# Kernel optimization log

Hardware: AMD Instinct MI355X
Metric: run time of the kernel (lower is better)

Reference implementation:

```python
import jax, jax.numpy as jnp
import numpy as np

GROUP = 32  # group_size from init


def setup_inputs() -> dict:
    key = jax.random.key(0)
    k1, k2, k3, k4, k5 = jax.random.split(key, 5)
    O, K = 4096, 4096
    B, S = 2, 2048
    num_groups = K // GROUP
    x = jax.random.normal(k1, (B, S, K), dtype=jnp.float32)
    # packed uint8 bytes (two 4-bit values per byte), stored as int32
    weight_packed = jax.random.randint(k2, (O, K // 2), 0, 256, dtype=jnp.int32)
    # realistic small positive scales and zero-points in [0, 15]
    scales = jax.random.uniform(k3, (O, num_groups), dtype=jnp.float32) * 0.02 + 1e-4
    zero_points = jax.random.uniform(k4, (O, num_groups), dtype=jnp.float32) * 15.0
    bias = jax.random.normal(k5, (O,), dtype=jnp.float32)
    return {"x": x, "weight_packed": weight_packed, "scales": scales,
            "zero_points": zero_points, "bias": bias}


def reference(x, weight_packed, scales, zero_points, bias):
    O, Kh = weight_packed.shape
    # unpack 4-bit values: even input index -> low nibble, odd -> high nibble
    low = weight_packed & 15
    high = (weight_packed >> 4) & 15
    q = jnp.stack([low, high], axis=-1).reshape(O, Kh * 2).astype(x.dtype)  # [O, K]
    # broadcast per-group scale/zero_point over the 32 elements of each group
    s = jnp.repeat(scales, GROUP, axis=1).astype(x.dtype)       # [O, K]
    z = jnp.repeat(zero_points, GROUP, axis=1).astype(x.dtype)  # [O, K]
    W = (q - z) * s  # dequantized weight [O, K]
    # F.linear: x @ W.T + bias
    return jnp.einsum('bsk,ok->bso', x, W) + bias
```

## Files before the change

kernel.cpp:

```cpp
#include <hip/hip_runtime.h>

typedef __attribute__((ext_vector_type(8))) short short8;
typedef __attribute__((ext_vector_type(4))) float f32x4;
typedef unsigned short u16;
typedef unsigned int u32;

#define BM 256
#define BN 256
#define BK 32
#define NBUF 4
#define LDP 40

__device__ __forceinline__ u16 f2bf_rne(float f) {
    u32 u = __float_as_uint(f);
    return (u16)((u + 0x7fffu + ((u >> 16) & 1u)) >> 16);
}
__device__ __forceinline__ float bf2f(u16 b) { return __uint_as_float(((u32)b) << 16); }


__global__ __launch_bounds__(256)
void prep_w(const int* __restrict__ WP, const float* __restrict__ S,
            const float* __restrict__ Z, u16* __restrict__ Wd, int NG)
{
    const int tid = blockIdx.x * blockDim.x + threadIdx.x;
    const int o = tid / NG, g = tid % NG;
    const float s = S[o * NG + g];
    const float nzs = -Z[o * NG + g] * s;
    const int4* p = (const int4*)&WP[(size_t)(o * NG + g) * 16];
    __align__(16) u16 out[32];
    #pragma unroll
    for (int q4 = 0; q4 < 4; ++q4) {
        const int4 v4 = p[q4];
        const int vv[4] = {v4.x, v4.y, v4.z, v4.w};
        #pragma unroll
        for (int j = 0; j < 4; ++j) {
            const int v = vv[j];
            out[(q4 * 4 + j) * 2]     = f2bf_rne(fmaf((float)(v & 15), s, nzs));
            out[(q4 * 4 + j) * 2 + 1] = f2bf_rne(fmaf((float)((v >> 4) & 15), s, nzs));
        }
    }
    uint4* dst = (uint4*)&Wd[(size_t)tid * 32];
    const uint4* src = (const uint4*)out;
    dst[0] = src[0]; dst[1] = src[1]; dst[2] = src[2]; dst[3] = src[3];
}

__global__ __launch_bounds__(256)
void prep_x(const float* __restrict__ X, u16* __restrict__ Xh)
{
    const int tid = blockIdx.x * blockDim.x + threadIdx.x;
    const float4 v0 = ((const float4*)X)[tid * 2];
    const float4 v1 = ((const float4*)X)[tid * 2 + 1];
    const float f[8] = {v0.x, v0.y, v0.z, v0.w, v1.x, v1.y, v1.z, v1.w};
    __align__(16) u16 h[8];
    #pragma unroll
    for (int j = 0; j < 8; ++j) h[j] = f2bf_rne(f[j]);
    ((uint4*)Xh)[tid] = *(uint4*)h;
}


#define GLDS(gptr, ldsbase)                                                         \
    __builtin_amdgcn_global_load_lds(                                               \
        (const __attribute__((address_space(1))) u32*)(gptr),                       \
        (__attribute__((address_space(3))) u32*)(ldsbase), 16, 0, 0)

__global__ __launch_bounds__(512, 2)
void gemm_q4(const u16* __restrict__ Xh, const u16* __restrict__ Wd,
             const float* __restrict__ Bi, float* __restrict__ C,
             int M, int N, int K)
{
    __shared__ __align__(16) u16 sA[NBUF * 8192];
    __shared__ __align__(16) u16 sB[NBUF * 8192];

    const int nbx = N / BN;
    const int nwg = gridDim.x;
    const int cpx = nwg >> 3;
    const int bid = blockIdx.x;
    const int swz = (bid & 7) * cpx + (bid >> 3);
    const int bx = swz % nbx, by = swz / nbx;
    const int brow = by * BM, bcol = bx * BN;

    const int t = threadIdx.x;
    const int lane = t & 63;
    const int wid = t >> 6;
    const int wr = wid >> 2;
    const int wcn = wid & 3;
    const int fr = lane & 15;
    const int ps8 = (((lane >> 4) ^ ((lane >> 2) & 3)) << 3);

    const int srow = wid * 16 + (lane >> 2);
    const int schunk = ((lane & 3) ^ ((lane >> 4) & 3)) * 8;
    const u16* srcA0 = Xh + (size_t)(brow + srow) * K + schunk;
    const u16* srcA1 = Xh + (size_t)(brow + 128 + srow) * K + schunk;
    const u16* srcB0 = Wd + (size_t)(bcol + srow) * K + schunk;
    const u16* srcB1 = Wd + (size_t)(bcol + 128 + srow) * K + schunk;

    f32x4 acc[8][4];
    #pragma unroll
    for (int m = 0; m < 8; ++m)
        #pragma unroll
        for (int n = 0; n < 4; ++n) acc[m][n] = (f32x4)0.f;

    const int nkt = K / BK;

#define STAGE(bufi, kt)                                                   \
    do {                                                                  \
        const size_t ko = (size_t)(kt) * BK;                              \
        char* baA = (char*)sA + (bufi) * 16384 + wid * 1024;              \
        char* baB = (char*)sB + (bufi) * 16384 + wid * 1024;              \
        GLDS(srcA0 + ko, baA);                                            \
        GLDS(srcA1 + ko, baA + 8192);                                     \
        GLDS(srcB0 + ko, baB);                                            \
        GLDS(srcB1 + ko, baB + 8192);                                     \
    } while (0)

    STAGE(0, 0);
    STAGE(1, 1);
    STAGE(2, 2);
    STAGE(3, 3);
    asm volatile("s_waitcnt vmcnt(12)" ::: "memory");
    __builtin_amdgcn_s_barrier();

    for (int kt = 0; kt < nkt; ++kt) {
        const int cur = kt & 3;
        const u16* bufA = sA + cur * 8192;
        const u16* bufB = sB + cur * 8192;

        short8 a[8], b[4];
        #pragma unroll
        for (int m = 0; m < 8; ++m) {
            const int row = wr * 128 + m * 16 + fr;
            a[m] = *(const short8*)&bufA[row * 32 + ps8];
        }
        #pragma unroll
        for (int n = 0; n < 4; ++n) {
            const int row = wcn * 64 + n * 16 + fr;
            b[n] = *(const short8*)&bufB[row * 32 + ps8];
        }

        asm volatile("s_waitcnt lgkmcnt(0)" ::: "memory");
        __builtin_amdgcn_s_barrier();

        if (kt + 4 < nkt) STAGE(cur, kt + 4);

        __builtin_amdgcn_s_setprio(1);
        #pragma unroll
        for (int m = 0; m < 8; ++m)
            #pragma unroll
            for (int n = 0; n < 4; ++n)
                acc[m][n] = __builtin_amdgcn_mfma_f32_16x16x32_bf16(a[m], b[n], acc[m][n], 0, 0, 0);
        __builtin_amdgcn_s_setprio(0);

        if (kt + 4 < nkt)      asm volatile("s_waitcnt vmcnt(12)" ::: "memory");
        else if (kt + 3 < nkt) asm volatile("s_waitcnt vmcnt(8)"  ::: "memory");
        else if (kt + 2 < nkt) asm volatile("s_waitcnt vmcnt(4)"  ::: "memory");
        else if (kt + 1 < nkt) asm volatile("s_waitcnt vmcnt(0)"  ::: "memory");
        __builtin_amdgcn_s_barrier();
    }

    const int row4 = (lane >> 4) << 2;
    const int col = lane & 15;
    #pragma unroll
    for (int n = 0; n < 4; ++n) {
        const int gc = bcol + wcn * 64 + n * 16 + col;
        const float bb = Bi[gc];
        #pragma unroll
        for (int m = 0; m < 8; ++m) {
            const int gr = brow + wr * 128 + m * 16 + row4;
            #pragma unroll
            for (int i = 0; i < 4; ++i)
                C[(size_t)(gr + i) * N + gc] = acc[m][n][i] + bb;
        }
    }
}
#undef STAGE
#undef GLDS


__global__ __launch_bounds__(256, 2)
void q4_gemm_fused(const float* __restrict__ X, const int* __restrict__ WP,
                   const float* __restrict__ S, const float* __restrict__ Z,
                   const float* __restrict__ Bi, float* __restrict__ C,
                   int M, int N, int K, int NG)
{
    __shared__ __align__(16) u16 sa_hi[128][LDP];
    __shared__ __align__(16) u16 sa_lo[128][LDP];
    __shared__ __align__(16) u16 sb_hi[128][LDP];
    __shared__ __align__(16) u16 sb_lo[128][LDP];

    const int nbx = N / 128;
    const int bx = blockIdx.x % nbx;
    const int by = blockIdx.x / nbx;
    const int brow = by * 128, bcol = bx * 128;

    const int t = threadIdx.x;
    const int lane = t & 63;
    const int wid = t >> 6;
    const int wr = wid >> 1, wc = wid & 1;
    const int xc4 = t & 7, xr0 = t >> 3;
    const int wrow = t >> 1, whalf = t & 1;
    const int Kh = K >> 1;

    f32x4 acc[4][4];
    #pragma unroll
    for (int m = 0; m < 4; ++m)
        #pragma unroll
        for (int n = 0; n < 4; ++n) acc[m][n] = (f32x4)0.f;

    const int fr = lane & 15;
    const int k8 = (lane >> 4) << 3;

    const int nkt = K / 32;
    for (int kt = 0; kt < nkt; ++kt) {
        #pragma unroll
        for (int p = 0; p < 4; ++p) {
            const int r = xr0 + p * 32;
            const float4 v = *(const float4*)&X[(size_t)(brow + r) * K + kt * 32 + xc4 * 4];
            u16 h[4], l[4];
            const float f[4] = {v.x, v.y, v.z, v.w};
            #pragma unroll
            for (int j = 0; j < 4; ++j) {
                h[j] = f2bf_rne(f[j]);
                l[j] = f2bf_rne(f[j] - bf2f(h[j]));
            }
            *(ushort4*)&sa_hi[r][xc4 * 4] = *(ushort4*)h;
            *(ushort4*)&sa_lo[r][xc4 * 4] = *(ushort4*)l;
        }
        {
            const int n = bcol + wrow;
            const float s = S[n * NG + kt];
            const float z = Z[n * NG + kt];
            const float nzs = -z * s;
            const int4* pp = (const int4*)&WP[(size_t)n * Kh + kt * 16 + whalf * 8];
            const int4 p0 = pp[0], p1 = pp[1];
            const int vals[8] = {p0.x, p0.y, p0.z, p0.w, p1.x, p1.y, p1.z, p1.w};
            __align__(16) u16 hi[16], lo[16];
            #pragma unroll
            for (int j = 0; j < 8; ++j) {
                const int v = vals[j];
                const float w0 = fmaf((float)(v & 15), s, nzs);
                const float w1 = fmaf((float)((v >> 4) & 15), s, nzs);
                hi[2 * j] = f2bf_rne(w0); lo[2 * j] = f2bf_rne(w0 - bf2f(hi[2 * j]));
                hi[2 * j + 1] = f2bf_rne(w1); lo[2 * j + 1] = f2bf_rne(w1 - bf2f(hi[2 * j + 1]));
            }
            #pragma unroll
            for (int q = 0; q < 4; ++q) {
                *(ushort4*)&sb_hi[wrow][whalf * 16 + q * 4] = *(ushort4*)&hi[q * 4];
                *(ushort4*)&sb_lo[wrow][whalf * 16 + q * 4] = *(ushort4*)&lo[q * 4];
            }
        }
        __syncthreads();

        short8 ah[4], al[4], bh[4], bl[4];
        #pragma unroll
        for (int m = 0; m < 4; ++m) {
            ah[m] = *(const short8*)&sa_hi[wr * 64 + m * 16 + fr][k8];
            al[m] = *(const short8*)&sa_lo[wr * 64 + m * 16 + fr][k8];
        }
        #pragma unroll
        for (int n = 0; n < 4; ++n) {
            bh[n] = *(const short8*)&sb_hi[wc * 64 + n * 16 + fr][k8];
            bl[n] = *(const short8*)&sb_lo[wc * 64 + n * 16 + fr][k8];
        }
        #pragma unroll
        for (int m = 0; m < 4; ++m)
            #pragma unroll
            for (int n = 0; n < 4; ++n) {
                acc[m][n] = __builtin_amdgcn_mfma_f32_16x16x32_bf16(ah[m], bh[n], acc[m][n], 0, 0, 0);
                acc[m][n] = __builtin_amdgcn_mfma_f32_16x16x32_bf16(ah[m], bl[n], acc[m][n], 0, 0, 0);
                acc[m][n] = __builtin_amdgcn_mfma_f32_16x16x32_bf16(al[m], bh[n], acc[m][n], 0, 0, 0);
            }
        __syncthreads();
    }

    const int row4 = (lane >> 4) << 2;
    const int col = lane & 15;
    #pragma unroll
    for (int n = 0; n < 4; ++n) {
        const int gc = bcol + wc * 64 + n * 16 + col;
        const float bb = Bi[gc];
        #pragma unroll
        for (int m = 0; m < 4; ++m) {
            const int gr = brow + wr * 64 + m * 16 + row4;
            #pragma unroll
            for (int i = 0; i < 4; ++i)
                C[(size_t)(gr + i) * N + gc] = acc[m][n][i] + bb;
        }
    }
}


extern "C" void kernel_launch(void* const* d_in, const int* in_sizes, int n_in,
                              void* d_out, int out_size, void* d_ws, size_t ws_size,
                              hipStream_t stream)
{
    const float* X  = (const float*)d_in[0];
    const int*   WP = (const int*)d_in[1];
    const float* S  = (const float*)d_in[2];
    const float* Z  = (const float*)d_in[3];
    const float* Bi = (const float*)d_in[4];
    float* C = (float*)d_out;

    const int O  = in_sizes[4];
    const int NG = in_sizes[2] / O;
    const int K  = NG * 32;
    const int M  = in_sizes[0] / K;

    const size_t needW = (size_t)O * K * 2;
    const size_t needX = (size_t)M * K * 2;
    const size_t need = needW + needX;

    if (ws_size >= need && (M % BM) == 0 && (O % BN) == 0) {
        u16* Wd  = (u16*)d_ws;
        u16* Xhp = Wd + (size_t)O * K;

        prep_w<<<(O * NG) / 256, 256, 0, stream>>>(WP, S, Z, Wd, NG);
        prep_x<<<(M * K / 8) / 256, 256, 0, stream>>>(X, Xhp);

        dim3 grid((M / BM) * (O / BN));
        gemm_q4<<<grid, 512, 0, stream>>>(Xhp, Wd, Bi, C, M, O, K);
    } else {
        dim3 grid((M / 128) * (O / 128));
        q4_gemm_fused<<<grid, 256, 0, stream>>>(X, WP, S, Z, Bi, C, M, O, K, NG);
    }
}
```

Measured before the change: 307.1 us.

## Prefetch next k-tile LDS fragments into registers during MFMA compute

```diff
diff --git a/kernel.cpp b/kernel.cpp
--- a/kernel.cpp
+++ b/kernel.cpp
@@ -113,34 +113,38 @@
         GLDS(srcB1 + ko, baB + 8192);                                     \
     } while (0)
 
+#define READ_FRAGS(dst_a, dst_b, bufi)                                    \
+    do {                                                                  \
+        const u16* _bA = sA + (bufi) * 8192;                              \
+        const u16* _bB = sB + (bufi) * 8192;                              \
+        _Pragma("unroll")                                                 \
+        for (int m = 0; m < 8; ++m) {                                     \
+            const int row = wr * 128 + m * 16 + fr;                       \
+            dst_a[m] = *(const short8*)&_bA[row * 32 + ps8];              \
+        }                                                                 \
+        _Pragma("unroll")                                                 \
+        for (int n = 0; n < 4; ++n) {                                     \
+            const int row = wcn * 64 + n * 16 + fr;                       \
+            dst_b[n] = *(const short8*)&_bB[row * 32 + ps8];              \
+        }                                                                 \
+    } while (0)
+
     STAGE(0, 0);
     STAGE(1, 1);
     STAGE(2, 2);
     STAGE(3, 3);
-    asm volatile("s_waitcnt vmcnt(12)" ::: "memory");
+    asm volatile("s_waitcnt vmcnt(8)" ::: "memory");
     __builtin_amdgcn_s_barrier();
+
+    short8 a[8], b[4];
+    READ_FRAGS(a, b, 0);
 
     for (int kt = 0; kt < nkt; ++kt) {
         const int cur = kt & 3;
-        const u16* bufA = sA + cur * 8192;
-        const u16* bufB = sB + cur * 8192;
-
-        short8 a[8], b[4];
-        #pragma unroll
-        for (int m = 0; m < 8; ++m) {
-            const int row = wr * 128 + m * 16 + fr;
-            a[m] = *(const short8*)&bufA[row * 32 + ps8];
-        }
-        #pragma unroll
-        for (int n = 0; n < 4; ++n) {
-            const int row = wcn * 64 + n * 16 + fr;
-            b[n] = *(const short8*)&bufB[row * 32 + ps8];
-        }
-
-        asm volatile("s_waitcnt lgkmcnt(0)" ::: "memory");
-        __builtin_amdgcn_s_barrier();
-
-        if (kt + 4 < nkt) STAGE(cur, kt + 4);
+        const int nxt = (kt + 1) & 3;
+
+        short8 na[8], nb[4];
+        if (kt + 1 < nkt) READ_FRAGS(na, nb, nxt);
 
         __builtin_amdgcn_s_setprio(1);
         #pragma unroll
@@ -149,11 +153,23 @@
             for (int n = 0; n < 4; ++n)
                 acc[m][n] = __builtin_amdgcn_mfma_f32_16x16x32_bf16(a[m], b[n], acc[m][n], 0, 0, 0);
         __builtin_amdgcn_s_setprio(0);
-
-        if (kt + 4 < nkt)      asm volatile("s_waitcnt vmcnt(12)" ::: "memory");
-        else if (kt + 3 < nkt) asm volatile("s_waitcnt vmcnt(8)"  ::: "memory");
-        else if (kt + 2 < nkt) asm volatile("s_waitcnt vmcnt(4)"  ::: "memory");
-        else if (kt + 1 < nkt) asm volatile("s_waitcnt vmcnt(0)"  ::: "memory");
+        __builtin_amdgcn_sched_barrier(0);
+
+        asm volatile("s_waitcnt lgkmcnt(0)" ::: "memory");
+        __builtin_amdgcn_s_barrier();
+
+        if (kt + 4 < nkt) STAGE(cur, kt + 4);
+
+        if (kt + 1 < nkt) {
+            #pragma unroll
+            for (int m = 0; m < 8; ++m) a[m] = na[m];
+            #pragma unroll
+            for (int n = 0; n < 4; ++n) b[n] = nb[n];
+        }
+
+        if (kt + 4 < nkt)      asm volatile("s_waitcnt vmcnt(8)" ::: "memory");
+        else if (kt + 3 < nkt) asm volatile("s_waitcnt vmcnt(4)" ::: "memory");
+        else                   asm volatile("s_waitcnt vmcnt(0)" ::: "memory");
         __builtin_amdgcn_s_barrier();
     }
 
@@ -172,6 +188,7 @@
         }
     }
 }
+#undef READ_FRAGS
 #undef STAGE
 #undef GLDS
 
```

Result: slower. 319.6 us (+4.0%).
